# Kernel optimization log

Hardware: AMD Instinct MI355X
Metric: run time of the kernel (lower is better)

The kernel has to match this reference:

```python
import jax, jax.numpy as jnp
import numpy as np

D = 6  # hardcoded feature dim from nn.Linear(6, 6)
NEG = -1000000.0


def setup_inputs() -> dict:
    key = jax.random.key(0)
    ks = jax.random.split(key, 8)
    B, S = 32, 2048
    X = jax.random.normal(ks[0], (B, S, D), dtype=jnp.float32)
    attention_mask = jax.random.randint(ks[1], (B, S), 0, 2).astype(jnp.int32)
    # torch nn.Linear params: weight [out,in], bias [out]
    lim = 1.0 / np.sqrt(D)
    Wq = jax.random.uniform(ks[2], (D, D), jnp.float32, -lim, lim)
    bq = jax.random.uniform(ks[3], (D,), jnp.float32, -lim, lim)
    Wk = jax.random.uniform(ks[4], (D, D), jnp.float32, -lim, lim)
    bk = jax.random.uniform(ks[5], (D,), jnp.float32, -lim, lim)
    Wv = jax.random.uniform(ks[6], (D, D), jnp.float32, -lim, lim)
    bv = jax.random.uniform(ks[7], (D,), jnp.float32, -lim, lim)
    return {"X": X, "attention_mask": attention_mask,
            "Wq": Wq, "bq": bq, "Wk": Wk, "bk": bk, "Wv": Wv, "bv": bv}


def reference(X, attention_mask, Wq, bq, Wk, bk, Wv, bv):
    # Linear projections (torch Linear: x @ W^T + b)
    Q = X @ Wq.T + bq  # [B,S,D]
    K = X @ Wk.T + bk
    V = X @ Wv.T + bv
    score = jnp.einsum('bsd,btd->bst', Q, K)  # [B,S,S]
    m1 = (attention_mask == 0)[:, :, None]  # mask rows
    m2 = (attention_mask == 0)[:, None, :]  # mask cols
    score = jnp.where(m1 | m2, NEG, score)
    weight = jax.nn.softmax(score, axis=-1)
    return jnp.einsum('bst,btd->bsd', weight, V)
```

## Files before the change

kernel.cpp:

```cpp
#include <hip/hip_runtime.h>

#define SEQ 2048
#define DIM 6
#define NW 8
#define BLOCK (NW * 64)
#define VROW 2056

typedef _Float16 half4F __attribute__((ext_vector_type(4)));
typedef short bf16x4 __attribute__((ext_vector_type(4)));
typedef float f32x4 __attribute__((ext_vector_type(4)));

union FragU { uint2 u; half4F h; bf16x4 b; };

__device__ __forceinline__ unsigned pkh(float a, float b) {
    return __builtin_bit_cast(unsigned, __builtin_amdgcn_cvt_pkrtz(a, b));
}
__device__ __forceinline__ unsigned bf16rn(float x) {
    unsigned u = __builtin_bit_cast(unsigned, x);
    return (u + 0x7FFFu + ((u >> 16) & 1u)) >> 16;
}
__device__ __forceinline__ unsigned pkbf_trunc(float a, float b) {
    return __builtin_amdgcn_perm(__builtin_bit_cast(unsigned, b),
                                 __builtin_bit_cast(unsigned, a),
                                 0x07060302u);
}

__device__ __forceinline__ f32x4 mfma_bf16_(bf16x4 a, bf16x4 b, f32x4 c) {
#if __has_builtin(__builtin_amdgcn_mfma_f32_16x16x16bf16_1k)
    return __builtin_amdgcn_mfma_f32_16x16x16bf16_1k(a, b, c, 0, 0, 0);
#else
    f32x4 d;
    asm("v_mfma_f32_16x16x16_bf16 %0, %1, %2, %3"
        : "=v"(d) : "v"(a), "v"(b), "v"(c));
    return d;
#endif
}


__launch_bounds__(BLOCK, 4)
__global__ void attn_mfma(const float* __restrict__ X,
                          const int* __restrict__ mask,
                          const float* __restrict__ Wq, const float* __restrict__ bq,
                          const float* __restrict__ Wk, const float* __restrict__ bk,
                          const float* __restrict__ Wv, const float* __restrict__ bv,
                          float* __restrict__ out) {
    __shared__ __align__(16) __fp16 Ksm[SEQ * 8];
    __shared__ __align__(16) unsigned short Vtsm[7 * VROW];

    const int b = blockIdx.x >> 4;
    const int tid = threadIdx.x;
    const float* Xb = X + (size_t)b * SEQ * DIM;
    const int* mb = mask + (size_t)b * SEQ;
    const float L2E = 1.44269504088896f;

#pragma unroll
    for (int i = 0; i < SEQ / BLOCK; ++i) {
        const int t = tid + i * BLOCK;
        const float2* xp = reinterpret_cast<const float2*>(Xb + t * DIM);
        float2 x01 = xp[0], x23 = xp[1], x45 = xp[2];
        float x[DIM] = {x01.x, x01.y, x23.x, x23.y, x45.x, x45.y};
        float kk[DIM], vv[DIM];
#pragma unroll
        for (int r = 0; r < DIM; ++r) {
            float k = bk[r], v = bv[r];
#pragma unroll
            for (int c = 0; c < DIM; ++c) {
                k = fmaf(Wk[r * DIM + c], x[c], k);
                v = fmaf(Wv[r * DIM + c], x[c], v);
            }
            kk[r] = k * L2E;
            vv[r] = v;
        }
        const float bias = (mb[t] == 0) ? -1024.0f : 0.0f;
        uint4 kw;
        kw.x = pkh(kk[0], kk[1]);
        kw.y = pkh(kk[2], kk[3]);
        kw.z = pkh(kk[4], kk[5]);
        kw.w = pkh(bias, 0.0f);
        *reinterpret_cast<uint4*>(&Ksm[t * 8]) = kw;
#pragma unroll
        for (int r = 0; r < DIM; ++r)
            Vtsm[r * VROW + t] = (unsigned short)bf16rn(vv[r]);
        Vtsm[6 * VROW + t] = 0x3F80u;
    }
    __syncthreads();

    const int lane = tid & 63, wid = tid >> 6;
    const int s0 = ((blockIdx.x & 15) * NW + wid) * 16;
    const int r15 = lane & 15, g = lane >> 4;
    const int s = s0 + r15;

    float qq[DIM], biasm;
    {
        const float2* xp = reinterpret_cast<const float2*>(Xb + s * DIM);
        float2 x01 = xp[0], x23 = xp[1], x45 = xp[2];
        float x[DIM] = {x01.x, x01.y, x23.x, x23.y, x45.x, x45.y};
        const bool rm = (mb[s] == 0);
#pragma unroll
        for (int r = 0; r < DIM; ++r) {
            float q = bq[r];
#pragma unroll
            for (int c = 0; c < DIM; ++c) q = fmaf(Wq[r * DIM + c], x[c], q);
            qq[r] = rm ? 0.0f : q;
        }
        biasm = rm ? 0.0f : 1.0f;
    }

    FragU qf;
    qf.u.x = (g == 0) ? pkh(qq[0], qq[1]) : (g == 1) ? pkh(qq[4], qq[5]) : 0u;
    qf.u.y = (g == 0) ? pkh(qq[2], qq[3]) : (g == 1) ? pkh(biasm, 0.0f) : 0u;

    const f32x4 zero4 = {0.0f, 0.0f, 0.0f, 0.0f};

    f32x4 acc = zero4;
    {
        const int dcl = (r15 < 6) ? r15 : 6;
        int kidx = r15 * 8 + (g & 1) * 4;
        int vidx = dcl * VROW + g * 4;
#pragma unroll 4
        for (int tt = 0; tt < SEQ / 16; ++tt) {
            half4F kf = *reinterpret_cast<const half4F*>(&Ksm[kidx]);
            bf16x4 vf = *reinterpret_cast<const bf16x4*>(&Vtsm[vidx]);
            f32x4 d = __builtin_amdgcn_mfma_f32_16x16x16f16(kf, qf.h, zero4, 0, 0, 0);
            FragU pa;
            pa.u.x = pkbf_trunc(__builtin_amdgcn_exp2f(d[0]),
                                __builtin_amdgcn_exp2f(d[1]));
            pa.u.y = pkbf_trunc(__builtin_amdgcn_exp2f(d[2]),
                                __builtin_amdgcn_exp2f(d[3]));
            acc = mfma_bf16_(pa.b, vf, acc);
            kidx += 128;
            vidx += 16;
        }
    }

    const int srcl = (lane & 48) | 6;
#pragma unroll
    for (int r = 0; r < 4; ++r) {
        const float dnm = __shfl(acc[r], srcl);
        const float val = acc[r] * __builtin_amdgcn_rcpf(dnm);
        if (r15 < 6) {
            out[((size_t)b * SEQ + s0 + g * 4 + r) * DIM + r15] = val;
        }
    }
}

extern "C" void kernel_launch(void* const* d_in, const int* in_sizes, int n_in,
                              void* d_out, int out_size, void* d_ws, size_t ws_size,
                              hipStream_t stream) {
    const float* X  = (const float*)d_in[0];
    const int* mask = (const int*)d_in[1];
    const float* Wq = (const float*)d_in[2];
    const float* bq = (const float*)d_in[3];
    const float* Wk = (const float*)d_in[4];
    const float* bk = (const float*)d_in[5];
    const float* Wv = (const float*)d_in[6];
    const float* bv = (const float*)d_in[7];
    float* out = (float*)d_out;

    const int B = in_sizes[0] / (SEQ * DIM);

    dim3 grid(B * 16);
    attn_mfma<<<grid, BLOCK, 0, stream>>>(X, mask, Wq, bq, Wk, bk, Wv, bv, out);
}
```

Measured before the change: 25.57 us.

## Compact unmasked keys and queries in a prep kernel to skip masked work

Adds a prep kernel that runs a per-batch prefix scan over the mask and writes compacted K/V for unmasked positions to workspace. It also writes the mean of V directly as the output for masked query rows. The attention kernel then loops only over the compacted keys and queries, so roughly half the keys and queries are skipped given the random mask. In exchange it adds a second launch, global workspace traffic, and indirect row scatter on the output.

```diff
diff --git a/kernel.cpp b/kernel.cpp
--- a/kernel.cpp
+++ b/kernel.cpp
@@ -2,8 +2,6 @@
 
 #define SEQ 2048
 #define DIM 6
-#define NW 8
-#define BLOCK (NW * 64)
 #define VROW 2056
 
 typedef _Float16 half4F __attribute__((ext_vector_type(4)));
@@ -37,25 +35,42 @@
 }
 
 
-__launch_bounds__(BLOCK, 4)
-__global__ void attn_mfma(const float* __restrict__ X,
-                          const int* __restrict__ mask,
-                          const float* __restrict__ Wq, const float* __restrict__ bq,
-                          const float* __restrict__ Wk, const float* __restrict__ bk,
-                          const float* __restrict__ Wv, const float* __restrict__ bv,
-                          float* __restrict__ out) {
-    __shared__ __align__(16) __fp16 Ksm[SEQ * 8];
-    __shared__ __align__(16) unsigned short Vtsm[7 * VROW];
-
-    const int b = blockIdx.x >> 4;
-    const int tid = threadIdx.x;
+__launch_bounds__(256)
+__global__ void prep(const float* __restrict__ X, const int* __restrict__ mask,
+                     const float* __restrict__ Wk, const float* __restrict__ bk,
+                     const float* __restrict__ Wv, const float* __restrict__ bv,
+                     __fp16* __restrict__ Kc, unsigned short* __restrict__ VcT,
+                     int* __restrict__ rowl, int* __restrict__ nuArr,
+                     float* __restrict__ out) {
+    __shared__ int sA[256], sB[256];
+    __shared__ float vsr[6][256];
+    const int b = blockIdx.x, tid = threadIdx.x;
     const float* Xb = X + (size_t)b * SEQ * DIM;
     const int* mb = mask + (size_t)b * SEQ;
     const float L2E = 1.44269504088896f;
 
-#pragma unroll
-    for (int i = 0; i < SEQ / BLOCK; ++i) {
-        const int t = tid + i * BLOCK;
+    const int t0 = tid * 8;
+    int mloc[8]; int c = 0;
+#pragma unroll
+    for (int j = 0; j < 8; ++j) { mloc[j] = (mb[t0 + j] != 0); c += mloc[j]; }
+    sA[tid] = c;
+    __syncthreads();
+    int* src = sA; int* dst = sB;
+    for (int off = 1; off < 256; off <<= 1) {
+        int v = src[tid];
+        if (tid >= off) v += src[tid - off];
+        dst[tid] = v;
+        __syncthreads();
+        int* tmp = src; src = dst; dst = tmp;
+    }
+    const int Nu = src[255];
+    int slot = src[tid] - c;
+    if (tid == 0) nuArr[b] = Nu;
+
+    float vsum[6] = {0, 0, 0, 0, 0, 0};
+#pragma unroll
+    for (int j = 0; j < 8; ++j) {
+        const int t = t0 + j;
         const float2* xp = reinterpret_cast<const float2*>(Xb + t * DIM);
         float2 x01 = xp[0], x23 = xp[1], x45 = xp[2];
         float x[DIM] = {x01.x, x01.y, x23.x, x23.y, x45.x, x45.y};
@@ -64,63 +79,125 @@
         for (int r = 0; r < DIM; ++r) {
             float k = bk[r], v = bv[r];
 #pragma unroll
-            for (int c = 0; c < DIM; ++c) {
-                k = fmaf(Wk[r * DIM + c], x[c], k);
-                v = fmaf(Wv[r * DIM + c], x[c], v);
+            for (int cc = 0; cc < DIM; ++cc) {
+                k = fmaf(Wk[r * DIM + cc], x[cc], k);
+                v = fmaf(Wv[r * DIM + cc], x[cc], v);
             }
             kk[r] = k * L2E;
             vv[r] = v;
-        }
-        const float bias = (mb[t] == 0) ? -1024.0f : 0.0f;
-        uint4 kw;
-        kw.x = pkh(kk[0], kk[1]);
-        kw.y = pkh(kk[2], kk[3]);
-        kw.z = pkh(kk[4], kk[5]);
-        kw.w = pkh(bias, 0.0f);
-        *reinterpret_cast<uint4*>(&Ksm[t * 8]) = kw;
-#pragma unroll
-        for (int r = 0; r < DIM; ++r)
-            Vtsm[r * VROW + t] = (unsigned short)bf16rn(vv[r]);
-        Vtsm[6 * VROW + t] = 0x3F80u;
-    }
+            vsum[r] += v;
+        }
+        if (mloc[j]) {
+            uint4 kw;
+            kw.x = pkh(kk[0], kk[1]);
+            kw.y = pkh(kk[2], kk[3]);
+            kw.z = pkh(kk[4], kk[5]);
+            kw.w = pkh(0.0f, 0.0f);
+            *reinterpret_cast<uint4*>(Kc + ((size_t)b * SEQ + slot) * 8) = kw;
+            unsigned short* vb = VcT + (size_t)b * 7 * SEQ + slot;
+#pragma unroll
+            for (int r = 0; r < DIM; ++r) vb[r * SEQ] = (unsigned short)bf16rn(vv[r]);
+            vb[6 * SEQ] = 0x3F80u;
+            rowl[(size_t)b * SEQ + slot] = t;
+            ++slot;
+        }
+    }
+    const int NT16 = (Nu + 15) & ~15;
+    if (tid < NT16 - Nu) {
+        const int s = Nu + tid;
+        uint4 kw; kw.x = 0; kw.y = 0; kw.z = 0; kw.w = pkh(-1024.0f, 0.0f);
+        *reinterpret_cast<uint4*>(Kc + ((size_t)b * SEQ + s) * 8) = kw;
+        unsigned short* vb = VcT + (size_t)b * 7 * SEQ + s;
+#pragma unroll
+        for (int r = 0; r < 7; ++r) vb[r * SEQ] = 0;
+    }
+#pragma unroll
+    for (int r = 0; r < DIM; ++r) vsr[r][tid] = vsum[r];
     __syncthreads();
+    for (int off = 128; off > 0; off >>= 1) {
+        if (tid < off) {
+#pragma unroll
+            for (int r = 0; r < DIM; ++r) vsr[r][tid] += vsr[r][tid + off];
+        }
+        __syncthreads();
+    }
+    float meanV[DIM];
+#pragma unroll
+    for (int r = 0; r < DIM; ++r) meanV[r] = vsr[r][0] * (1.0f / SEQ);
+#pragma unroll
+    for (int j = 0; j < 8; ++j) {
+        if (!mloc[j]) {
+            float* o = out + ((size_t)b * SEQ + t0 + j) * DIM;
+            o[0] = meanV[0]; o[1] = meanV[1]; o[2] = meanV[2];
+            o[3] = meanV[3]; o[4] = meanV[4]; o[5] = meanV[5];
+        }
+    }
+}
+
+__launch_bounds__(256, 2)
+__global__ void attn_mfma(const float* __restrict__ X,
+                          const float* __restrict__ Wq, const float* __restrict__ bq,
+                          const __fp16* __restrict__ Kc,
+                          const unsigned short* __restrict__ VcT,
+                          const int* __restrict__ rowl, const int* __restrict__ nuArr,
+                          float* __restrict__ out) {
+    __shared__ __align__(16) __fp16 Ksm[SEQ * 8];
+    __shared__ __align__(16) unsigned short Vt[7 * VROW];
+
+    const int b = blockIdx.x >> 5, sc = blockIdx.x & 31;
+    const int tid = threadIdx.x;
+    const int Nu = nuArr[b];
+    const int s_base = sc * 64;
+    if (s_base >= Nu) return;
+    const int NT16 = (Nu + 15) & ~15;
+
+    const uint4* ks = reinterpret_cast<const uint4*>(Kc + (size_t)b * SEQ * 8);
+    for (int i = tid; i < NT16; i += 256)
+        reinterpret_cast<uint4*>(Ksm)[i] = ks[i];
+    const int nch = NT16 >> 3;
+    for (int i = tid; i < 7 * nch; i += 256) {
+        const int r = i / nch, cc = i - r * nch;
+        *reinterpret_cast<uint4*>(&Vt[r * VROW + cc * 8]) =
+            *reinterpret_cast<const uint4*>(&VcT[((size_t)b * 7 + r) * SEQ + cc * 8]);
+    }
+    __syncthreads();
 
     const int lane = tid & 63, wid = tid >> 6;
-    const int s0 = ((blockIdx.x & 15) * NW + wid) * 16;
+    const int s0 = s_base + wid * 16;
+    if (s0 >= Nu) return;
     const int r15 = lane & 15, g = lane >> 4;
-    const int s = s0 + r15;
-
-    float qq[DIM], biasm;
+    const int sidx = s0 + r15;
+    const int srow = rowl[(size_t)b * SEQ + (sidx < Nu ? sidx : Nu - 1)];
+
+    const float* Xb = X + (size_t)b * SEQ * DIM;
+    float qq[DIM];
     {
-        const float2* xp = reinterpret_cast<const float2*>(Xb + s * DIM);
+        const float2* xp = reinterpret_cast<const float2*>(Xb + srow * DIM);
         float2 x01 = xp[0], x23 = xp[1], x45 = xp[2];
         float x[DIM] = {x01.x, x01.y, x23.x, x23.y, x45.x, x45.y};
-        const bool rm = (mb[s] == 0);
 #pragma unroll
         for (int r = 0; r < DIM; ++r) {
             float q = bq[r];
 #pragma unroll
-            for (int c = 0; c < DIM; ++c) q = fmaf(Wq[r * DIM + c], x[c], q);
-            qq[r] = rm ? 0.0f : q;
-        }
-        biasm = rm ? 0.0f : 1.0f;
-    }
-
+            for (int cc = 0; cc < DIM; ++cc) q = fmaf(Wq[r * DIM + cc], x[cc], q);
+            qq[r] = q;
+        }
+    }
     FragU qf;
     qf.u.x = (g == 0) ? pkh(qq[0], qq[1]) : (g == 1) ? pkh(qq[4], qq[5]) : 0u;
-    qf.u.y = (g == 0) ? pkh(qq[2], qq[3]) : (g == 1) ? pkh(biasm, 0.0f) : 0u;
+    qf.u.y = (g == 0) ? pkh(qq[2], qq[3]) : (g == 1) ? pkh(1.0f, 0.0f) : 0u;
 
     const f32x4 zero4 = {0.0f, 0.0f, 0.0f, 0.0f};
-
     f32x4 acc = zero4;
+    const int ntiles = NT16 >> 4;
     {
         const int dcl = (r15 < 6) ? r15 : 6;
         int kidx = r15 * 8 + (g & 1) * 4;
         int vidx = dcl * VROW + g * 4;
-#pragma unroll 4
-        for (int tt = 0; tt < SEQ / 16; ++tt) {
+#pragma unroll 2
+        for (int tt = 0; tt < ntiles; ++tt) {
             half4F kf = *reinterpret_cast<const half4F*>(&Ksm[kidx]);
-            bf16x4 vf = *reinterpret_cast<const bf16x4*>(&Vtsm[vidx]);
+            bf16x4 vf = *reinterpret_cast<const bf16x4*>(&Vt[vidx]);
             f32x4 d = __builtin_amdgcn_mfma_f32_16x16x16f16(kf, qf.h, zero4, 0, 0, 0);
             FragU pa;
             pa.u.x = pkbf_trunc(__builtin_amdgcn_exp2f(d[0]),
@@ -138,8 +215,10 @@
     for (int r = 0; r < 4; ++r) {
         const float dnm = __shfl(acc[r], srcl);
         const float val = acc[r] * __builtin_amdgcn_rcpf(dnm);
-        if (r15 < 6) {
-            out[((size_t)b * SEQ + s0 + g * 4 + r) * DIM + r15] = val;
+        const int oidx = s0 + g * 4 + r;
+        if (r15 < 6 && oidx < Nu) {
+            const int orow = rowl[(size_t)b * SEQ + oidx];
+            out[((size_t)b * SEQ + orow) * DIM + r15] = val;
         }
     }
 }
@@ -159,6 +238,12 @@
 
     const int B = in_sizes[0] / (SEQ * DIM);
 
-    dim3 grid(B * 16);
-    attn_mfma<<<grid, BLOCK, 0, stream>>>(X, mask, Wq, bq, Wk, bk, Wv, bv, out);
-}
+    __fp16* Kc = (__fp16*)d_ws;
+    unsigned short* VcT = (unsigned short*)(Kc + (size_t)B * SEQ * 8);
+    int* rowl = (int*)(VcT + (size_t)B * 7 * SEQ);
+    int* nuArr = rowl + (size_t)B * SEQ;
+
+    prep<<<dim3(B), 256, 0, stream>>>(X, mask, Wk, bk, Wv, bv,
+                                      Kc, VcT, rowl, nuArr, out);
+    attn_mfma<<<dim3(B * 32), 256, 0, stream>>>(X, Wq, bq, Kc, VcT, rowl, nuArr, out);
+}
```

Measured after the change: 37.89 us. 1.48x slower.

## Compact unmasked keys and rows in a prep kernel to skip masked attention work

Applied to the files above, without the earlier changes.

A new prep kernel computes K and V once per batch, runs a prefix scan over the mask, and writes only the unmasked keys and values into compacted workspace buffers, together with a map from slot to original row and per-segment V sums. The attention kernel then loops only over the unmasked key tiles and only over unmasked query rows. Fully masked rows get the uniform mean of V, computed from the precomputed sums. This removes roughly half the MFMA and exp work for a random mask and avoids recomputing K/V in all 16 blocks of each batch. In exchange it adds a second kernel launch, a global-memory round trip for K/V, and scattered output writes through the row map.

```diff
diff --git a/kernel.cpp b/kernel.cpp
--- a/kernel.cpp
+++ b/kernel.cpp
@@ -2,8 +2,8 @@
 
 #define SEQ 2048
 #define DIM 6
-#define NW 8
-#define BLOCK (NW * 64)
+#define NSEG 8
+#define SEGR (SEQ / NSEG)
 #define VROW 2056
 
 typedef _Float16 half4F __attribute__((ext_vector_type(4)));
@@ -18,6 +18,9 @@
 __device__ __forceinline__ unsigned bf16rn(float x) {
     unsigned u = __builtin_bit_cast(unsigned, x);
     return (u + 0x7FFFu + ((u >> 16) & 1u)) >> 16;
+}
+__device__ __forceinline__ unsigned pkbf(float a, float b) {
+    return bf16rn(a) | (bf16rn(b) << 16);
 }
 __device__ __forceinline__ unsigned pkbf_trunc(float a, float b) {
     return __builtin_amdgcn_perm(__builtin_bit_cast(unsigned, b),
@@ -37,90 +40,180 @@
 }
 
 
-__launch_bounds__(BLOCK, 4)
-__global__ void attn_mfma(const float* __restrict__ X,
-                          const int* __restrict__ mask,
-                          const float* __restrict__ Wq, const float* __restrict__ bq,
-                          const float* __restrict__ Wk, const float* __restrict__ bk,
-                          const float* __restrict__ Wv, const float* __restrict__ bv,
-                          float* __restrict__ out) {
-    __shared__ __align__(16) __fp16 Ksm[SEQ * 8];
-    __shared__ __align__(16) unsigned short Vtsm[7 * VROW];
-
-    const int b = blockIdx.x >> 4;
+__launch_bounds__(256)
+__global__ void prep(const float* __restrict__ X, const int* __restrict__ mask,
+                     const float* __restrict__ Wk, const float* __restrict__ bk,
+                     const float* __restrict__ Wv, const float* __restrict__ bv,
+                     __fp16* __restrict__ Kc, unsigned short* __restrict__ Vc,
+                     unsigned short* __restrict__ rowl,
+                     float* __restrict__ vsumP, int* __restrict__ nuArr) {
+    __shared__ unsigned char msk[SEQ];
+    __shared__ int sA[256], sB[256];
+    __shared__ float vred[4][8];
+    const int b = blockIdx.x >> 3, seg = blockIdx.x & 7;
     const int tid = threadIdx.x;
-    const float* Xb = X + (size_t)b * SEQ * DIM;
     const int* mb = mask + (size_t)b * SEQ;
     const float L2E = 1.44269504088896f;
 
-#pragma unroll
-    for (int i = 0; i < SEQ / BLOCK; ++i) {
-        const int t = tid + i * BLOCK;
-        const float2* xp = reinterpret_cast<const float2*>(Xb + t * DIM);
-        float2 x01 = xp[0], x23 = xp[1], x45 = xp[2];
-        float x[DIM] = {x01.x, x01.y, x23.x, x23.y, x45.x, x45.y};
-        float kk[DIM], vv[DIM];
-#pragma unroll
-        for (int r = 0; r < DIM; ++r) {
-            float k = bk[r], v = bv[r];
-#pragma unroll
-            for (int c = 0; c < DIM; ++c) {
-                k = fmaf(Wk[r * DIM + c], x[c], k);
-                v = fmaf(Wv[r * DIM + c], x[c], v);
-            }
-            kk[r] = k * L2E;
-            vv[r] = v;
-        }
-        const float bias = (mb[t] == 0) ? -1024.0f : 0.0f;
+    int cnt = 0;
+#pragma unroll
+    for (int j = 0; j < 8; ++j) {
+        const int m = (mb[tid * 8 + j] != 0);
+        msk[tid * 8 + j] = (unsigned char)m;
+        cnt += m;
+    }
+    sA[tid] = cnt;
+    __syncthreads();
+    int* src = sA; int* dst = sB;
+    for (int off = 1; off < 256; off <<= 1) {
+        int v = src[tid];
+        if (tid >= off) v += src[tid - off];
+        dst[tid] = v;
+        __syncthreads();
+        int* tmp = src; src = dst; dst = tmp;
+    }
+    if (seg == 0 && tid == 0) nuArr[b] = src[255];
+
+    const int t = seg * SEGR + tid;
+    const int i8 = t >> 3;
+    int slot = (i8 > 0) ? src[i8 - 1] : 0;
+    for (int j = i8 * 8; j < t; ++j) slot += msk[j];
+
+    const float2* xp = reinterpret_cast<const float2*>(X + ((size_t)b * SEQ + t) * DIM);
+    float2 x01 = xp[0], x23 = xp[1], x45 = xp[2];
+    float x[DIM] = {x01.x, x01.y, x23.x, x23.y, x45.x, x45.y};
+    float kk[DIM], vv[DIM];
+#pragma unroll
+    for (int r = 0; r < DIM; ++r) {
+        float k = bk[r], v = bv[r];
+#pragma unroll
+        for (int c = 0; c < DIM; ++c) {
+            k = fmaf(Wk[r * DIM + c], x[c], k);
+            v = fmaf(Wv[r * DIM + c], x[c], v);
+        }
+        kk[r] = k * L2E;
+        vv[r] = v;
+    }
+    if (msk[t]) {
         uint4 kw;
         kw.x = pkh(kk[0], kk[1]);
         kw.y = pkh(kk[2], kk[3]);
         kw.z = pkh(kk[4], kk[5]);
-        kw.w = pkh(bias, 0.0f);
-        *reinterpret_cast<uint4*>(&Ksm[t * 8]) = kw;
-#pragma unroll
-        for (int r = 0; r < DIM; ++r)
-            Vtsm[r * VROW + t] = (unsigned short)bf16rn(vv[r]);
-        Vtsm[6 * VROW + t] = 0x3F80u;
+        kw.w = 0u;
+        *reinterpret_cast<uint4*>(Kc + ((size_t)b * SEQ + slot) * 8) = kw;
+        uint4 vw;
+        vw.x = pkbf(vv[0], vv[1]);
+        vw.y = pkbf(vv[2], vv[3]);
+        vw.z = pkbf(vv[4], vv[5]);
+        vw.w = 0u;
+        *reinterpret_cast<uint4*>(Vc + ((size_t)b * SEQ + slot) * 8) = vw;
+        rowl[(size_t)b * SEQ + slot] = (unsigned short)t;
+    }
+
+    const int lane = tid & 63, wid = tid >> 6;
+#pragma unroll
+    for (int r = 0; r < DIM; ++r) {
+        float s = vv[r];
+#pragma unroll
+        for (int off = 1; off < 64; off <<= 1) s += __shfl_xor(s, off);
+        if (lane == 0) vred[wid][r] = s;
     }
     __syncthreads();
+    if (tid < DIM) {
+        vsumP[((size_t)b * NSEG + seg) * 8 + tid] =
+            vred[0][tid] + vred[1][tid] + vred[2][tid] + vred[3][tid];
+    }
+}
+
+__launch_bounds__(512, 2)
+__global__ void attn_mfma(const float* __restrict__ X,
+                          const int* __restrict__ mask,
+                          const float* __restrict__ Wq, const float* __restrict__ bq,
+                          const __fp16* __restrict__ Kc,
+                          const unsigned short* __restrict__ Vc,
+                          const unsigned short* __restrict__ rowl,
+                          const float* __restrict__ vsumP,
+                          const int* __restrict__ nuArr,
+                          float* __restrict__ out) {
+    __shared__ __align__(16) __fp16 Ksm[SEQ * 8];
+    __shared__ __align__(16) unsigned short Vt[7 * VROW];
+
+    const int b = blockIdx.x >> 4, blk = blockIdx.x & 15;
+    const int tid = threadIdx.x;
+    const int Nu = nuArr[b];
+
+    if (tid < 128) {
+        const int t = blk * 128 + tid;
+        if (mask[(size_t)b * SEQ + t] == 0) {
+            float* o = out + ((size_t)b * SEQ + t) * DIM;
+#pragma unroll
+            for (int r = 0; r < DIM; ++r) {
+                float s = 0.0f;
+#pragma unroll
+                for (int g2 = 0; g2 < NSEG; ++g2)
+                    s += vsumP[((size_t)b * NSEG + g2) * 8 + r];
+                o[r] = s * (1.0f / SEQ);
+            }
+        }
+    }
+
+    const int rowbase = blk * 128;
+    if (rowbase >= Nu) return;
+    const int NT16 = (Nu + 15) & ~15;
+
+    const uint4* kg = reinterpret_cast<const uint4*>(Kc + (size_t)b * SEQ * 8);
+    const uint4* vg = reinterpret_cast<const uint4*>(Vc + (size_t)b * SEQ * 8);
+    for (int i = tid; i < NT16; i += 512) {
+        uint4 kw, vw;
+        if (i < Nu) { kw = kg[i]; vw = vg[i]; }
+        else { kw = make_uint4(0, 0, 0, pkh(-1024.0f, 0.0f)); vw = make_uint4(0, 0, 0, 0); }
+        reinterpret_cast<uint4*>(Ksm)[i] = kw;
+        Vt[0 * VROW + i] = (unsigned short)(vw.x & 0xFFFFu);
+        Vt[1 * VROW + i] = (unsigned short)(vw.x >> 16);
+        Vt[2 * VROW + i] = (unsigned short)(vw.y & 0xFFFFu);
+        Vt[3 * VROW + i] = (unsigned short)(vw.y >> 16);
+        Vt[4 * VROW + i] = (unsigned short)(vw.z & 0xFFFFu);
+        Vt[5 * VROW + i] = (unsigned short)(vw.z >> 16);
+        Vt[6 * VROW + i] = (i < Nu) ? 0x3F80u : 0u;
+    }
+    __syncthreads();
 
     const int lane = tid & 63, wid = tid >> 6;
-    const int s0 = ((blockIdx.x & 15) * NW + wid) * 16;
+    const int s0 = rowbase + wid * 16;
+    if (s0 >= Nu) return;
     const int r15 = lane & 15, g = lane >> 4;
-    const int s = s0 + r15;
-
-    float qq[DIM], biasm;
+    const int sidx = s0 + r15;
+    const int srow = rowl[(size_t)b * SEQ + (sidx < Nu ? sidx : Nu - 1)];
+
+    float qq[DIM];
     {
-        const float2* xp = reinterpret_cast<const float2*>(Xb + s * DIM);
+        const float2* xp =
+            reinterpret_cast<const float2*>(X + ((size_t)b * SEQ + srow) * DIM);
         float2 x01 = xp[0], x23 = xp[1], x45 = xp[2];
         float x[DIM] = {x01.x, x01.y, x23.x, x23.y, x45.x, x45.y};
-        const bool rm = (mb[s] == 0);
 #pragma unroll
         for (int r = 0; r < DIM; ++r) {
             float q = bq[r];
 #pragma unroll
             for (int c = 0; c < DIM; ++c) q = fmaf(Wq[r * DIM + c], x[c], q);
-            qq[r] = rm ? 0.0f : q;
-        }
-        biasm = rm ? 0.0f : 1.0f;
-    }
-
+            qq[r] = q;
+        }
+    }
     FragU qf;
     qf.u.x = (g == 0) ? pkh(qq[0], qq[1]) : (g == 1) ? pkh(qq[4], qq[5]) : 0u;
-    qf.u.y = (g == 0) ? pkh(qq[2], qq[3]) : (g == 1) ? pkh(biasm, 0.0f) : 0u;
+    qf.u.y = (g == 0) ? pkh(qq[2], qq[3]) : (g == 1) ? pkh(1.0f, 0.0f) : 0u;
 
     const f32x4 zero4 = {0.0f, 0.0f, 0.0f, 0.0f};
-
     f32x4 acc = zero4;
     {
         const int dcl = (r15 < 6) ? r15 : 6;
         int kidx = r15 * 8 + (g & 1) * 4;
         int vidx = dcl * VROW + g * 4;
+        const int ntiles = NT16 >> 4;
 #pragma unroll 4
-        for (int tt = 0; tt < SEQ / 16; ++tt) {
+        for (int tt = 0; tt < ntiles; ++tt) {
             half4F kf = *reinterpret_cast<const half4F*>(&Ksm[kidx]);
-            bf16x4 vf = *reinterpret_cast<const bf16x4*>(&Vtsm[vidx]);
+            bf16x4 vf = *reinterpret_cast<const bf16x4*>(&Vt[vidx]);
             f32x4 d = __builtin_amdgcn_mfma_f32_16x16x16f16(kf, qf.h, zero4, 0, 0, 0);
             FragU pa;
             pa.u.x = pkbf_trunc(__builtin_amdgcn_exp2f(d[0]),
@@ -138,8 +231,10 @@
     for (int r = 0; r < 4; ++r) {
         const float dnm = __shfl(acc[r], srcl);
         const float val = acc[r] * __builtin_amdgcn_rcpf(dnm);
-        if (r15 < 6) {
-            out[((size_t)b * SEQ + s0 + g * 4 + r) * DIM + r15] = val;
+        const int oidx = s0 + g * 4 + r;
+        if (r15 < 6 && oidx < Nu) {
+            const int orow = rowl[(size_t)b * SEQ + oidx];
+            out[((size_t)b * SEQ + orow) * DIM + r15] = val;
         }
     }
 }
@@ -159,6 +254,14 @@
 
     const int B = in_sizes[0] / (SEQ * DIM);
 
-    dim3 grid(B * 16);
-    attn_mfma<<<grid, BLOCK, 0, stream>>>(X, mask, Wq, bq, Wk, bk, Wv, bv, out);
-}
+    __fp16* Kc = (__fp16*)d_ws;
+    unsigned short* Vc = (unsigned short*)(Kc + (size_t)B * SEQ * 8);
+    unsigned short* rowl = Vc + (size_t)B * SEQ * 8;
+    float* vsumP = (float*)(rowl + (size_t)B * SEQ);
+    int* nuArr = (int*)(vsumP + (size_t)B * NSEG * 8);
+
+    prep<<<dim3(B * NSEG), 256, 0, stream>>>(X, mask, Wk, bk, Wv, bv,
+                                             Kc, Vc, rowl, vsumP, nuArr);
+    attn_mfma<<<dim3(B * 16), 512, 0, stream>>>(X, mask, Wq, bq, Kc, Vc, rowl,
+                                                vsumP, nuArr, out);
+}
```

Result: faster. 24.01 us (-6.1%).
